# Performance work log

Hardware: AMD Instinct MI355X
Metric: run time of the kernel (lower is better)

## Reference

```python
import jax, jax.numpy as jnp
import numpy as np
import math

D_MODEL = 1024
EPS = 1e-6  # RMSNorm epsilon


def setup_inputs() -> dict:
    key = jax.random.key(0)
    ks = jax.random.split(key, 9)
    d = D_MODEL
    B, T = 4, 4096
    s = 1.0 / math.sqrt(d)
    return {
        "x": jax.random.normal(ks[0], (B, T, d), dtype=jnp.float32),
        "w_key": jax.random.normal(ks[1], (2 * d, d), dtype=jnp.float32) * s,  # Linear(d, 2d, bias=False)
        "conv_w": jax.random.normal(ks[2], (d, 1, 3), dtype=jnp.float32) * (1.0 / math.sqrt(3)),  # depthwise k=3
        "conv_b": jax.random.normal(ks[3], (d,), dtype=jnp.float32) * 0.02,
        "w1": jax.random.normal(ks[4], (2 * d, d), dtype=jnp.float32) * s,  # Linear(d, 2d)
        "b1": jax.random.normal(ks[5], (2 * d,), dtype=jnp.float32) * 0.02,
        "w2": jax.random.normal(ks[6], (d, 2 * d), dtype=jnp.float32) * (1.0 / math.sqrt(2 * d)),  # Linear(2d, d)
        "b2": jax.random.normal(ks[7], (d,), dtype=jnp.float32) * 0.02,
        "norm_w": jnp.ones((d,), dtype=jnp.float32),
    }


def parallel_lerp_scan(theta, alpha):
    # h_t = lerp(h_{t-1}, theta_t, alpha_t) = (1-alpha_t)*h_{t-1} + alpha_t*theta_t
    # Linear recurrence h_t = a_t*h_{t-1} + b_t -> log-depth associative scan.
    a = 1.0 - alpha
    b = alpha * theta

    def combine(c1, c2):
        a1, b1 = c1
        a2, b2 = c2
        return (a2 * a1, a2 * b1 + b2)

    _, h = jax.lax.associative_scan(combine, (a, b), axis=1)
    return h


def rms_norm(x, w):
    var = jnp.mean(jnp.square(x), axis=-1, keepdims=True)
    return x * jax.lax.rsqrt(var + EPS) * w


def reference(x, w_key, conv_w, conv_b, w1, b1, w2, b2, norm_w):
    d = x.shape[-1]
    res = jnp.einsum('btd,ed->bte', x, w_key)  # [B,T,2D]
    theta, alpha = res[..., :d], res[..., d:]
    h = parallel_lerp_scan(jnp.tanh(theta) * math.pi, jax.nn.sigmoid(alpha))
    h = h.astype(x.dtype)
    # causal depthwise conv: left-pad (k-1)=2 zeros along time
    h_t = jnp.transpose(h, (0, 2, 1))  # [B,D,T]
    conv = jax.lax.conv_general_dilated(
        h_t, conv_w, window_strides=(1,), padding=[(2, 0)],
        feature_group_count=d, dimension_numbers=('NCH', 'OIH', 'NCH'))
    h_bound = jnp.transpose(conv + conv_b[None, :, None], (0, 2, 1))  # [B,T,D]
    z = h + h_bound
    hid = jax.nn.silu(jnp.einsum('btd,ed->bte', z, w1) + b1)
    h_final = jnp.einsum('bte,de->btd', hid, w2) + b2
    return rms_norm(h_final, norm_w)
```

## Files before the change

### kernel.cpp

```cpp
#include <hip/hip_runtime.h>

typedef unsigned short u16;
typedef unsigned int u32;
typedef __attribute__((ext_vector_type(8))) short short8;
typedef __attribute__((ext_vector_type(4))) float f32x4;

#define T_LEN 4096
#define BATCH 4
#define M_TOT (BATCH*T_LEN)
#define NCHUNK 32
#define CLEN 128

__device__ __forceinline__ u16 f2bf(float f){
  u32 u = __builtin_bit_cast(u32, f);
  u32 r = (u + 0x7FFFu + ((u >> 16) & 1u)) >> 16;
  return (u16)r;
}
__device__ __forceinline__ float bf2f(u16 h){
  u32 u = ((u32)h) << 16; return __builtin_bit_cast(float, u);
}
__device__ __forceinline__ float sigmoid_(float v){ return 1.f/(1.f + __expf(-v)); }
__device__ __forceinline__ float tanh_pi_(float v){
  return 3.14159265358979323846f * (1.f - 2.f/(1.f + __expf(2.f*v)));
}

__global__ __launch_bounds__(256) void cvt_bf16_k(const float* __restrict__ in,
                                                  u16* __restrict__ out, int n4){
  int g = blockIdx.x*256 + threadIdx.x;
  if (g >= n4) return;
  float4 v = reinterpret_cast<const float4*>(in)[g];
  reinterpret_cast<ushort4*>(out)[g] =
      make_ushort4(f2bf(v.x), f2bf(v.y), f2bf(v.z), f2bf(v.w));
}

#define BAR() __builtin_amdgcn_s_barrier()
#define WAITLGKM0() asm volatile("s_waitcnt lgkmcnt(0)" ::: "memory")
#define VMCNT(n) asm volatile("s_waitcnt vmcnt(" #n ")" ::: "memory")

#define STAGE(buf, ab, q, kt) do { \
  const u16* _s = ((ab) ? Bb : Ab) + (size_t)(q)*rowK64 + (size_t)(kt)*64; \
  __builtin_amdgcn_global_load_lds( \
    (const __attribute__((address_space(1))) void*)_s, \
    (__attribute__((address_space(3))) void*)(smem + (buf)*65536 + (ab)*32768 + (q)*8192 + stb), \
    16, 0, 0); \
} while(0)

#define LDA(buf, m, kk) (*(const short8*)(smem + (buf)*65536 + aRow + (m)*2048 + ((kk) ? csw1 : csw0)))
#define LDB(buf, n, kk) (*(const short8*)(smem + (buf)*65536 + 32768 + bRow + (n)*2048 + ((kk) ? csw1 : csw0)))

#define PFA(dst, buf, q) do { \
  dst[0] = LDA(buf, 2*(q),   0); \
  dst[1] = LDA(buf, 2*(q),   1); \
  dst[2] = LDA(buf, 2*(q)+1, 0); \
  dst[3] = LDA(buf, 2*(q)+1, 1); } while(0)

#define PFB(d0, d1, buf) do { _Pragma("unroll") \
  for (int n=0;n<4;n++){ d0[n] = LDB(buf,n,0); d1[n] = LDB(buf,n,1); } } while(0)

#define MFMA_Q(q, A, B0, B1) do { _Pragma("unroll") \
  for (int n=0;n<4;n++){ \
    acc[2*(q)][n]   = __builtin_amdgcn_mfma_f32_16x16x32_bf16(A[0], B0[n], acc[2*(q)][n], 0,0,0); \
    acc[2*(q)][n]   = __builtin_amdgcn_mfma_f32_16x16x32_bf16(A[1], B1[n], acc[2*(q)][n], 0,0,0); \
    acc[2*(q)+1][n] = __builtin_amdgcn_mfma_f32_16x16x32_bf16(A[2], B0[n], acc[2*(q)+1][n], 0,0,0); \
    acc[2*(q)+1][n] = __builtin_amdgcn_mfma_f32_16x16x32_bf16(A[3], B1[n], acc[2*(q)+1][n], 0,0,0); \
  } } while(0)

#define PRIO1() __builtin_amdgcn_s_setprio(1)
#define PRIO0() __builtin_amdgcn_s_setprio(0)

template<int EPI>
__global__ __launch_bounds__(512, 2) void gemm8p(
    const u16* __restrict__ Ag, const u16* __restrict__ Bg,
    const float* __restrict__ bias, void* __restrict__ Cout,
    int M, int N, int K)
{
  extern __shared__ __attribute__((aligned(16))) char smem[];
  const int tid = threadIdx.x;
  const int wid = tid >> 6, lane = tid & 63;
  const int wr = wid >> 2, wc = wid & 3;
  const int fr = lane & 15, fq = lane >> 4;

  const int nbn = N >> 8;
  const int nwg = gridDim.x;
  const int bid = blockIdx.x;
  const int swzb = (bid & 7) * (nwg >> 3) + (bid >> 3);
  const int bm = swzb / nbn, bn = swzb - bm * nbn;

  const size_t rowK64 = (size_t)64 * K;
  const u16* Ab = Ag + ((size_t)bm*256 + (tid>>3)) * K + ((tid & 7) ^ ((tid >> 3) & 7)) * 8;
  const u16* Bb = Bg + ((size_t)bn*256 + (tid>>3)) * K + ((tid & 7) ^ ((tid >> 3) & 7)) * 8;
  const u32 stb = (u32)(wid << 10);

  const u32 aRow = (u32)(wr*128 + fr) * 128;
  const u32 bRow = (u32)(wc*64  + fr) * 128;
  const u32 csw0 = (u32)((fq*16)      ^ ((fr & 7) << 4));
  const u32 csw1 = (u32)((64 + fq*16) ^ ((fr & 7) << 4));

  f32x4 acc[8][4];
#pragma unroll
  for (int m=0;m<8;m++)
#pragma unroll
    for (int n=0;n<4;n++) acc[m][n] = f32x4{0.f,0.f,0.f,0.f};

  short8 bP0[4], bP1[4], bN0[4], bN1[4];
  short8 aP[4], aN[4];

  const int NT = K >> 6;

  STAGE(0,1,0,0); STAGE(0,1,1,0); STAGE(0,1,2,0); STAGE(0,1,3,0);
  STAGE(0,0,0,0); STAGE(0,0,1,0); STAGE(0,0,2,0); STAGE(0,0,3,0);
  STAGE(1,1,0,1); STAGE(1,1,1,1); STAGE(1,1,2,1); STAGE(1,1,3,1);
  STAGE(1,0,0,1); STAGE(1,0,2,1);
  VMCNT(6);
  BAR();
  PFB(bP0, bP1, 0);
  PFA(aP, 0, 0);

  for (int i = 0; i < (NT>>1) - 1; ++i){
    const int tt = 2*i;
    STAGE(1,0,1,tt+1); STAGE(1,0,3,tt+1);
    BAR(); WAITLGKM0();
    PRIO1(); MFMA_Q(0, aP, bP0, bP1); PFA(aN, 0, 1); PRIO0();
    BAR();
    STAGE(0,1,0,tt+2); STAGE(0,1,1,tt+2);
    BAR(); WAITLGKM0();
    PRIO1(); MFMA_Q(1, aN, bP0, bP1); PFA(aP, 0, 2); PRIO0();
    BAR();
    STAGE(0,1,2,tt+2); STAGE(0,1,3,tt+2);
    BAR(); WAITLGKM0();
    PRIO1(); MFMA_Q(2, aP, bP0, bP1); PFA(aN, 0, 3); PRIO0();
    BAR();
    STAGE(0,0,0,tt+2); STAGE(0,0,2,tt+2);
    BAR(); WAITLGKM0(); VMCNT(6);
    PRIO1(); MFMA_Q(3, aN, bP0, bP1); PFB(bN0, bN1, 1); PFA(aP, 1, 0); PRIO0();
    BAR();
    STAGE(0,0,1,tt+2); STAGE(0,0,3,tt+2);
    BAR(); WAITLGKM0();
    PRIO1(); MFMA_Q(0, aP, bN0, bN1); PFA(aN, 1, 1); PRIO0();
    BAR();
    STAGE(1,1,0,tt+3); STAGE(1,1,1,tt+3);
    BAR(); WAITLGKM0();
    PRIO1(); MFMA_Q(1, aN, bN0, bN1); PFA(aP, 1, 2); PRIO0();
    BAR();
    STAGE(1,1,2,tt+3); STAGE(1,1,3,tt+3);
    BAR(); WAITLGKM0();
    PRIO1(); MFMA_Q(2, aP, bN0, bN1); PFA(aN, 1, 3); PRIO0();
    BAR();
    STAGE(1,0,0,tt+3); STAGE(1,0,2,tt+3);
    BAR(); WAITLGKM0(); VMCNT(6);
    PRIO1(); MFMA_Q(3, aN, bN0, bN1); PFB(bP0, bP1, 0); PFA(aP, 0, 0); PRIO0();
    BAR();
  }
  {
    STAGE(1,0,1,NT-1); STAGE(1,0,3,NT-1);
    BAR(); WAITLGKM0();
    PRIO1(); MFMA_Q(0, aP, bP0, bP1); PFA(aN, 0, 1); PRIO0();
    BAR();
    BAR(); WAITLGKM0();
    PRIO1(); MFMA_Q(1, aN, bP0, bP1); PFA(aP, 0, 2); PRIO0();
    BAR();
    BAR(); WAITLGKM0();
    PRIO1(); MFMA_Q(2, aP, bP0, bP1); PFA(aN, 0, 3); PRIO0();
    BAR();
    BAR(); WAITLGKM0(); VMCNT(0);
    PRIO1(); MFMA_Q(3, aN, bP0, bP1); PFB(bN0, bN1, 1); PFA(aP, 1, 0); PRIO0();
    BAR();
    BAR(); WAITLGKM0();
    PRIO1(); MFMA_Q(0, aP, bN0, bN1); PFA(aN, 1, 1); PRIO0();
    BAR();
    BAR(); WAITLGKM0();
    PRIO1(); MFMA_Q(1, aN, bN0, bN1); PFA(aP, 1, 2); PRIO0();
    BAR();
    BAR(); WAITLGKM0();
    PRIO1(); MFMA_Q(2, aP, bN0, bN1); PFA(aN, 1, 3); PRIO0();
    BAR();
    BAR(); WAITLGKM0();
    PRIO1(); MFMA_Q(3, aN, bN0, bN1); PRIO0();
  }

  const int orow0 = bm*256 + wr*128;
  const int ocol0 = bn*256 + wc*64;
#pragma unroll
  for (int m=0;m<8;m++){
#pragma unroll
    for (int n=0;n<4;n++){
      const int col = ocol0 + n*16 + fr;
#pragma unroll
      for (int r=0;r<4;r++){
        const int row = orow0 + m*16 + fq*4 + r;
        float v = acc[m][n][r];
        if constexpr (EPI == 0){
          float o = (col < 1024) ? tanh_pi_(v) : sigmoid_(v);
          ((u16*)Cout)[(size_t)row*N + col] = f2bf(o);
        } else if constexpr (EPI == 1){
          v += bias[col];
          ((u16*)Cout)[(size_t)row*N + col] = f2bf(v * sigmoid_(v));
        } else {
          v += bias[col];
          ((float*)Cout)[(size_t)row*N + col] = v;
        }
      }
    }
  }
}

__global__ __launch_bounds__(256) void scan_stage1(const u16* __restrict__ res,
                                                   float* __restrict__ sA,
                                                   float* __restrict__ sB,
                                                   float* __restrict__ sA2,
                                                   float* __restrict__ sB2){
  const int c     = (blockIdx.x & 3)*256 + threadIdx.x;
  const int chunk = (blockIdx.x >> 2) & (NCHUNK-1);
  const int b     = blockIdx.x >> 7;
  const u16* p = res + ((size_t)(b*T_LEN + chunk*CLEN))*2048 + c;
  float A = 1.f, Bv = 0.f;
#pragma unroll 4
  for (int t=0;t<CLEN-1;++t){
    float th = bf2f(p[0]);
    float s  = bf2f(p[1024]);
    float a  = 1.f - s;
    A  *= a;
    Bv  = a*Bv + s*th;
    p  += 2048;
  }
  const int idx = (b*NCHUNK + chunk)*1024 + c;
  sA2[idx] = A; sB2[idx] = Bv;
  {
    float th = bf2f(p[0]);
    float s  = bf2f(p[1024]);
    float a  = 1.f - s;
    A  *= a;
    Bv  = a*Bv + s*th;
  }
  sA[idx] = A; sB[idx] = Bv;
}

__global__ __launch_bounds__(256) void scan_stage2(const float* __restrict__ sA,
                                                   const float* __restrict__ sB,
                                                   float* __restrict__ Hp){
  const int g = blockIdx.x*256 + threadIdx.x;
  const int b = g >> 10, c = g & 1023;
  float H = 0.f;
#pragma unroll
  for (int i=0;i<NCHUNK;++i){
    const int idx = (b*NCHUNK + i)*1024 + c;
    Hp[idx] = H;
    H = sA[idx]*H + sB[idx];
  }
}

__global__ __launch_bounds__(256) void scan3_conv_k(const u16* __restrict__ res,
                                                    const float* __restrict__ Hp,
                                                    const float* __restrict__ sA2,
                                                    const float* __restrict__ sB2,
                                                    const float* __restrict__ cw,
                                                    const float* __restrict__ cb,
                                                    u16* __restrict__ z){
  const int c     = (blockIdx.x & 3)*256 + threadIdx.x;
  const int chunk = (blockIdx.x >> 2) & (NCHUNK-1);
  const int b     = blockIdx.x >> 7;
  const u16* p = res + ((size_t)(b*T_LEN + chunk*CLEN))*2048 + c;
  u16*       q = z   + ((size_t)(b*T_LEN + chunk*CLEN))*1024 + c;
  const int idx = (b*NCHUNK + chunk)*1024 + c;
  float H   = Hp[idx];
  float hm1 = H;
  float hm2 = 0.f;
  if (chunk > 0){
    const int pidx = idx - 1024;
    hm2 = sA2[pidx]*Hp[pidx] + sB2[pidx];
  }
  const float w0 = cw[3*c], w1 = cw[3*c+1], w2 = cw[3*c+2], bb = cb[c];
#pragma unroll 4
  for (int t=0;t<CLEN;++t){
    float th = bf2f(p[0]);
    float s  = bf2f(p[1024]);
    H = (1.f - s)*H + s*th;
    float v = H + bb + hm2*w0 + hm1*w1 + H*w2;
    q[0] = f2bf(v);
    hm2 = hm1; hm1 = H;
    p += 2048; q += 1024;
  }
}

__global__ __launch_bounds__(256) void rmsnorm_k(float* __restrict__ io,
                                                 const float* __restrict__ w){
  const int row = blockIdx.x;
  const int tid = threadIdx.x;
  float* p = io + (size_t)row*1024;
  float4 v = reinterpret_cast<const float4*>(p)[tid];
  float ss = v.x*v.x + v.y*v.y + v.z*v.z + v.w*v.w;
#pragma unroll
  for (int o=32; o>0; o>>=1) ss += __shfl_xor(ss, o, 64);
  __shared__ float red[4];
  if ((tid & 63) == 0) red[tid >> 6] = ss;
  __syncthreads();
  float tot = red[0] + red[1] + red[2] + red[3];
  float scale = rsqrtf(tot * (1.f/1024.f) + 1e-6f);
  float4 wv = reinterpret_cast<const float4*>(w)[tid];
  float4 o;
  o.x = v.x*scale*wv.x; o.y = v.y*scale*wv.y;
  o.z = v.z*scale*wv.z; o.w = v.w*scale*wv.w;
  reinterpret_cast<float4*>(p)[tid] = o;
}

extern "C" void kernel_launch(void* const* d_in, const int* in_sizes, int n_in,
                              void* d_out, int out_size, void* d_ws, size_t ws_size,
                              hipStream_t stream) {
  const float* x      = (const float*)d_in[0];
  const float* w_key  = (const float*)d_in[1];
  const float* conv_w = (const float*)d_in[2];
  const float* conv_b = (const float*)d_in[3];
  const float* w1     = (const float*)d_in[4];
  const float* b1     = (const float*)d_in[5];
  const float* w2     = (const float*)d_in[6];
  const float* b2     = (const float*)d_in[7];
  const float* norm_w = (const float*)d_in[8];
  float* out = (float*)d_out;
  char*  ws  = (char*)d_ws;

  size_t off = 0;
  u16*   RES  = (u16*)  (ws + off); off += (size_t)M_TOT*2048*2;
  u16*   XB   = (u16*)  (ws + off); off += (size_t)M_TOT*1024*2;
  u16*   WK   = (u16*)  (ws + off); off += (size_t)2048*1024*2;
  u16*   W1B  = (u16*)  (ws + off); off += (size_t)2048*1024*2;
  u16*   W2B  = (u16*)  (ws + off); off += (size_t)1024*2048*2;
  float* SA   = (float*)(ws + off); off += (size_t)BATCH*NCHUNK*1024*4;
  float* SB   = (float*)(ws + off); off += (size_t)BATCH*NCHUNK*1024*4;
  float* SA2  = (float*)(ws + off); off += (size_t)BATCH*NCHUNK*1024*4;
  float* SB2  = (float*)(ws + off); off += (size_t)BATCH*NCHUNK*1024*4;
  float* HP   = (float*)(ws + off); off += (size_t)BATCH*NCHUNK*1024*4;
  u16* ZB  = XB;
  u16* HID = RES;

  hipFuncSetAttribute((const void*)gemm8p<0>, hipFuncAttributeMaxDynamicSharedMemorySize, 131072);
  hipFuncSetAttribute((const void*)gemm8p<1>, hipFuncAttributeMaxDynamicSharedMemorySize, 131072);
  hipFuncSetAttribute((const void*)gemm8p<2>, hipFuncAttributeMaxDynamicSharedMemorySize, 131072);

  cvt_bf16_k<<<(M_TOT*1024/4 + 255)/256, 256, 0, stream>>>(x,     XB,  M_TOT*1024/4);
  cvt_bf16_k<<<(2048*1024/4  + 255)/256, 256, 0, stream>>>(w_key, WK,  2048*1024/4);
  cvt_bf16_k<<<(2048*1024/4  + 255)/256, 256, 0, stream>>>(w1,    W1B, 2048*1024/4);
  cvt_bf16_k<<<(1024*2048/4  + 255)/256, 256, 0, stream>>>(w2,    W2B, 1024*2048/4);

  gemm8p<0><<<(M_TOT/256)*(2048/256), 512, 131072, stream>>>(XB, WK, nullptr, RES, M_TOT, 2048, 1024);

  scan_stage1<<<BATCH*NCHUNK*4, 256, 0, stream>>>(RES, SA, SB, SA2, SB2);
  scan_stage2<<<16, 256, 0, stream>>>(SA, SB, HP);
  scan3_conv_k<<<BATCH*NCHUNK*4, 256, 0, stream>>>(RES, HP, SA2, SB2, conv_w, conv_b, ZB);

  gemm8p<1><<<(M_TOT/256)*(2048/256), 512, 131072, stream>>>(ZB, W1B, b1, HID, M_TOT, 2048, 1024);

  gemm8p<2><<<(M_TOT/256)*(1024/256), 512, 131072, stream>>>(HID, W2B, b2, out, M_TOT, 1024, 2048);

  rmsnorm_k<<<M_TOT, 256, 0, stream>>>(out, norm_w);
}
```

Baseline: 316.8 us.

## Interleave LDS fragment prefetch with MFMAs using sched_group_barrier

Each phase of the GEMM main loop now issues the LDS fragment loads for the next step before the current step's MFMAs. sched_group_barrier hints ask the compiler to interleave those reads with the MFMAs, and the explicit lgkmcnt(0) waits are removed. The B-fragment prefetch is split into two halves spread across adjacent phases, with an extra vmcnt wait added so the staged data is ready. The aim is to hide LDS read latency behind matrix math instead of stalling after each MFMA block. The cost is more live registers and reliance on the compiler inserting correct waits, which could add stalls or register pressure.

```diff
diff --git a/kernel.cpp b/kernel.cpp
--- a/kernel.cpp
+++ b/kernel.cpp
@@ -34,8 +34,11 @@
 }
 
 #define BAR() __builtin_amdgcn_s_barrier()
-#define WAITLGKM0() asm volatile("s_waitcnt lgkmcnt(0)" ::: "memory")
 #define VMCNT(n) asm volatile("s_waitcnt vmcnt(" #n ")" ::: "memory")
+#define PRIO1() __builtin_amdgcn_s_setprio(1)
+#define PRIO0() __builtin_amdgcn_s_setprio(0)
+#define SGBPIN(R) do { __builtin_amdgcn_sched_group_barrier(0x100, R, 0); \
+                       __builtin_amdgcn_sched_group_barrier(0x008, 16, 0); } while(0)
 
 #define STAGE(buf, ab, q, kt) do { \
   const u16* _s = ((ab) ? Bb : Ab) + (size_t)(q)*rowK64 + (size_t)(kt)*64; \
@@ -54,8 +57,13 @@
   dst[2] = LDA(buf, 2*(q)+1, 0); \
   dst[3] = LDA(buf, 2*(q)+1, 1); } while(0)
 
-#define PFB(d0, d1, buf) do { _Pragma("unroll") \
-  for (int n=0;n<4;n++){ d0[n] = LDB(buf,n,0); d1[n] = LDB(buf,n,1); } } while(0)
+#define PFBH(d0, d1, buf, half) do { \
+  d0[2*(half)]   = LDB(buf, 2*(half),   0); \
+  d1[2*(half)]   = LDB(buf, 2*(half),   1); \
+  d0[2*(half)+1] = LDB(buf, 2*(half)+1, 0); \
+  d1[2*(half)+1] = LDB(buf, 2*(half)+1, 1); } while(0)
+
+#define PFB(d0, d1, buf) do { PFBH(d0,d1,buf,0); PFBH(d0,d1,buf,1); } while(0)
 
 #define MFMA_Q(q, A, B0, B1) do { _Pragma("unroll") \
   for (int n=0;n<4;n++){ \
@@ -64,9 +72,6 @@
     acc[2*(q)+1][n] = __builtin_amdgcn_mfma_f32_16x16x32_bf16(A[2], B0[n], acc[2*(q)+1][n], 0,0,0); \
     acc[2*(q)+1][n] = __builtin_amdgcn_mfma_f32_16x16x32_bf16(A[3], B1[n], acc[2*(q)+1][n], 0,0,0); \
   } } while(0)
-
-#define PRIO1() __builtin_amdgcn_s_setprio(1)
-#define PRIO0() __builtin_amdgcn_s_setprio(0)
 
 template<int EPI>
 __global__ __launch_bounds__(512, 2) void gemm8p(
@@ -119,62 +124,66 @@
   for (int i = 0; i < (NT>>1) - 1; ++i){
     const int tt = 2*i;
     STAGE(1,0,1,tt+1); STAGE(1,0,3,tt+1);
-    BAR(); WAITLGKM0();
-    PRIO1(); MFMA_Q(0, aP, bP0, bP1); PFA(aN, 0, 1); PRIO0();
+    BAR();
+    PRIO1(); PFA(aN,0,1); MFMA_Q(0, aP, bP0, bP1); PRIO0(); SGBPIN(4);
     BAR();
     STAGE(0,1,0,tt+2); STAGE(0,1,1,tt+2);
-    BAR(); WAITLGKM0();
-    PRIO1(); MFMA_Q(1, aN, bP0, bP1); PFA(aP, 0, 2); PRIO0();
+    BAR();
+    PRIO1(); PFA(aP,0,2); MFMA_Q(1, aN, bP0, bP1); PRIO0(); SGBPIN(4);
     BAR();
     STAGE(0,1,2,tt+2); STAGE(0,1,3,tt+2);
-    BAR(); WAITLGKM0();
-    PRIO1(); MFMA_Q(2, aP, bP0, bP1); PFA(aN, 0, 3); PRIO0();
+    BAR();
+    PRIO1(); PFA(aN,0,3); MFMA_Q(2, aP, bP0, bP1); PRIO0(); SGBPIN(4);
     BAR();
     STAGE(0,0,0,tt+2); STAGE(0,0,2,tt+2);
-    BAR(); WAITLGKM0(); VMCNT(6);
-    PRIO1(); MFMA_Q(3, aN, bP0, bP1); PFB(bN0, bN1, 1); PFA(aP, 1, 0); PRIO0();
+    BAR();
+    VMCNT(6);
+    PRIO1(); PFA(aP,1,0); PFBH(bN0,bN1,1,0); MFMA_Q(3, aN, bP0, bP1); PRIO0(); SGBPIN(8);
     BAR();
     STAGE(0,0,1,tt+2); STAGE(0,0,3,tt+2);
-    BAR(); WAITLGKM0();
-    PRIO1(); MFMA_Q(0, aP, bN0, bN1); PFA(aN, 1, 1); PRIO0();
+    BAR();
+    PRIO1(); PFBH(bN0,bN1,1,1); PFA(aN,1,1); MFMA_Q(0, aP, bN0, bN1); PRIO0(); SGBPIN(8);
     BAR();
     STAGE(1,1,0,tt+3); STAGE(1,1,1,tt+3);
-    BAR(); WAITLGKM0();
-    PRIO1(); MFMA_Q(1, aN, bN0, bN1); PFA(aP, 1, 2); PRIO0();
+    BAR();
+    PRIO1(); PFA(aP,1,2); MFMA_Q(1, aN, bN0, bN1); PRIO0(); SGBPIN(4);
     BAR();
     STAGE(1,1,2,tt+3); STAGE(1,1,3,tt+3);
-    BAR(); WAITLGKM0();
-    PRIO1(); MFMA_Q(2, aP, bN0, bN1); PFA(aN, 1, 3); PRIO0();
+    BAR();
+    VMCNT(8);
+    PRIO1(); PFA(aN,1,3); PFBH(bP0,bP1,0,0); MFMA_Q(2, aP, bN0, bN1); PRIO0(); SGBPIN(8);
     BAR();
     STAGE(1,0,0,tt+3); STAGE(1,0,2,tt+3);
-    BAR(); WAITLGKM0(); VMCNT(6);
-    PRIO1(); MFMA_Q(3, aN, bN0, bN1); PFB(bP0, bP1, 0); PFA(aP, 0, 0); PRIO0();
+    BAR();
+    VMCNT(6);
+    PRIO1(); PFA(aP,0,0); PFBH(bP0,bP1,0,1); MFMA_Q(3, aN, bN0, bN1); PRIO0(); SGBPIN(8);
     BAR();
   }
   {
     STAGE(1,0,1,NT-1); STAGE(1,0,3,NT-1);
-    BAR(); WAITLGKM0();
-    PRIO1(); MFMA_Q(0, aP, bP0, bP1); PFA(aN, 0, 1); PRIO0();
-    BAR();
-    BAR(); WAITLGKM0();
-    PRIO1(); MFMA_Q(1, aN, bP0, bP1); PFA(aP, 0, 2); PRIO0();
-    BAR();
-    BAR(); WAITLGKM0();
-    PRIO1(); MFMA_Q(2, aP, bP0, bP1); PFA(aN, 0, 3); PRIO0();
-    BAR();
-    BAR(); WAITLGKM0(); VMCNT(0);
-    PRIO1(); MFMA_Q(3, aN, bP0, bP1); PFB(bN0, bN1, 1); PFA(aP, 1, 0); PRIO0();
-    BAR();
-    BAR(); WAITLGKM0();
-    PRIO1(); MFMA_Q(0, aP, bN0, bN1); PFA(aN, 1, 1); PRIO0();
-    BAR();
-    BAR(); WAITLGKM0();
-    PRIO1(); MFMA_Q(1, aN, bN0, bN1); PFA(aP, 1, 2); PRIO0();
-    BAR();
-    BAR(); WAITLGKM0();
-    PRIO1(); MFMA_Q(2, aP, bN0, bN1); PFA(aN, 1, 3); PRIO0();
-    BAR();
-    BAR(); WAITLGKM0();
+    BAR();
+    PRIO1(); PFA(aN,0,1); MFMA_Q(0, aP, bP0, bP1); PRIO0(); SGBPIN(4);
+    BAR();
+    BAR();
+    PRIO1(); PFA(aP,0,2); MFMA_Q(1, aN, bP0, bP1); PRIO0(); SGBPIN(4);
+    BAR();
+    BAR();
+    PRIO1(); PFA(aN,0,3); MFMA_Q(2, aP, bP0, bP1); PRIO0(); SGBPIN(4);
+    BAR();
+    BAR();
+    VMCNT(0);
+    PRIO1(); PFA(aP,1,0); PFBH(bN0,bN1,1,0); MFMA_Q(3, aN, bP0, bP1); PRIO0(); SGBPIN(8);
+    BAR();
+    BAR();
+    PRIO1(); PFBH(bN0,bN1,1,1); PFA(aN,1,1); MFMA_Q(0, aP, bN0, bN1); PRIO0(); SGBPIN(8);
+    BAR();
+    BAR();
+    PRIO1(); PFA(aP,1,2); MFMA_Q(1, aN, bN0, bN1); PRIO0(); SGBPIN(4);
+    BAR();
+    BAR();
+    PRIO1(); PFA(aN,1,3); MFMA_Q(2, aP, bN0, bN1); PRIO0(); SGBPIN(4);
+    BAR();
+    BAR();
     PRIO1(); MFMA_Q(3, aN, bN0, bN1); PRIO0();
   }
 
```

After: 314.5 us. Within noise of the previous version (-0.7%).
